# Kernel tuning notes

Hardware: AMD Instinct MI355X
Metric: run time of the kernel (lower is better)

## Reference

```python
import jax, jax.numpy as jnp
import numpy as np

BN_EPS = 1e-5
LRELU_SLOPE = 0.2  # CBL = Conv1d(k=1) + BatchNorm1d + LeakyReLU


def three_nn(xyz1, xyz2):
    # xyz1: (B,N,3), xyz2: (B,M,3) -> squared dists (B,N,3), idx (B,N,3)
    d2 = (jnp.sum(xyz1 ** 2, -1, keepdims=True)
          + jnp.sum(xyz2 ** 2, -1)[:, None, :]
          - 2.0 * jnp.einsum('bnd,bmd->bnm', xyz1, xyz2))  # (B,N,M)
    neg, idx = jax.lax.top_k(-d2, 3)
    return -neg, idx


def three_interpolate(points2, idx, weight):
    # points2: (B,C,M), idx: (B,N,3), weight: (B,N,3) -> (B,C,N)
    gathered = jax.vmap(lambda p, i: p[:, i])(points2, idx)  # (B,C,N,3)
    return jnp.einsum('bcnk,bnk->bcn', gathered, weight)


def cbl(x, W, b, gamma, beta):
    # x: (B,C,N); 1x1 conv -> BN (training-mode stats) -> LeakyReLU
    y = jnp.einsum('oc,bcn->bon', W, x) + b[None, :, None]
    mean = jnp.mean(y, axis=(0, 2), keepdims=True)
    var = jnp.var(y, axis=(0, 2), keepdims=True)
    y = (y - mean) * jax.lax.rsqrt(var + BN_EPS)
    y = gamma[None, :, None] * y + beta[None, :, None]
    return jnp.where(y >= 0, y, LRELU_SLOPE * y)


def setup_inputs() -> dict:
    key = jax.random.key(0)
    ks = jax.random.split(key, 8)
    B, N, M = 4, 8192, 2048
    C1, C2 = 128, 256
    Cin = C2 + C1  # use_points1=True -> concat
    H = 256
    return {
        'xyz1': jax.random.normal(ks[0], (B, N, 3), jnp.float32),
        'xyz2': jax.random.normal(ks[1], (B, M, 3), jnp.float32),
        'points1': jax.random.normal(ks[2], (B, C1, N), jnp.float32),
        'points2': jax.random.normal(ks[3], (B, C2, M), jnp.float32),
        'W1': jax.random.normal(ks[4], (H, Cin), jnp.float32) * (1.0 / np.sqrt(Cin)),
        'b1': jnp.zeros((H,), jnp.float32),
        'gamma1': jnp.ones((H,), jnp.float32),
        'beta1': jnp.zeros((H,), jnp.float32),
        'W2': jax.random.normal(ks[5], (H, H), jnp.float32) * (1.0 / np.sqrt(H)),
        'b2': jnp.zeros((H,), jnp.float32),
        'gamma2': jnp.ones((H,), jnp.float32),
        'beta2': jnp.zeros((H,), jnp.float32),
    }


def reference(xyz1, xyz2, points1, points2, W1, b1, gamma1, beta1, W2, b2, gamma2, beta2):
    dist, idx = three_nn(xyz1, xyz2)
    dist = jnp.maximum(dist, 1e-10)
    recip = 1.0 / dist
    weight = recip / jnp.sum(recip, axis=2, keepdims=True)  # (B,N,3)
    interp = three_interpolate(points2, idx, weight)        # (B,C2,N)
    new_points = jnp.concatenate([interp, points1], axis=1)  # (B,C2+C1,N)
    new_points = cbl(new_points, W1, b1, gamma1, beta1)
    new_points = cbl(new_points, W2, b2, gamma2, beta2)
    return new_points
```

## Files before the change

kernel.cpp:

```cpp
#include <hip/hip_runtime.h>
#include <math.h>

constexpr int B   = 4;
constexpr int N   = 8192;
constexpr int M   = 2048;
constexpr int C1  = 128;
constexpr int C2  = 256;
constexpr int HCH = 256;
constexpr int CIN = 384;
constexpr float BN_EPS = 1e-5f;
constexpr float SLOPE  = 0.2f;
constexpr float BN_CNT = (float)(B * N);

typedef __attribute__((ext_vector_type(8))) short short8;
typedef __attribute__((ext_vector_type(4))) float f32x4;

__device__ __forceinline__ unsigned short bfh(float x) {
  unsigned int u = __float_as_uint(x);
  return (unsigned short)((u + 0x7fffu + ((u >> 16) & 1u)) >> 16);
}
__device__ __forceinline__ float bf2f(unsigned short h) {
  return __uint_as_float((unsigned int)h << 16);
}
__device__ __forceinline__ unsigned int pk(unsigned short a, unsigned short b) {
  return (unsigned int)a | ((unsigned int)b << 16);
}

__global__ void k_zero(float* __restrict__ stats) {
  int i = blockIdx.x * blockDim.x + threadIdx.x;
  if (i < 1024) stats[i] = 0.f;
}

__global__ __launch_bounds__(256) void k_nn(const float* __restrict__ xyz1,
                                            const float* __restrict__ xyz2,
                                            float* __restrict__ wgt,
                                            int* __restrict__ idxo) {
  __shared__ float4 q[4][512];
  __shared__ float  md[4][64][3];
  __shared__ int    mi[4][64][3];
  const int tid = threadIdx.x;
  const int b   = blockIdx.y;
  const int n0  = blockIdx.x * 64;

  const float* src = xyz2 + (size_t)b * M * 3;
  for (int i = tid; i < M; i += 256) {
    float x = src[i*3+0], y = src[i*3+1], z = src[i*3+2];
    q[i >> 9][i & 511] = make_float4(x, y, z, x*x + y*y + z*z);
  }
  __syncthreads();

  const int w = tid >> 6;
  const int t = tid & 63;
  const int n = n0 + t;
  const float* p = xyz1 + ((size_t)b * N + n) * 3;
  const float px = p[0], py = p[1], pz = p[2];
  const float n1 = px*px + py*py + pz*pz;

  float d0 = 3.4e38f, d1 = 3.4e38f, d2 = 3.4e38f;
  int   j0 = 0, j1 = 0, j2 = 0;
  const float4* qs = q[w];
  #pragma unroll 4
  for (int r = 0; r < 512; ++r) {
    float4 c = qs[r];
    float dot = px*c.x + py*c.y + pz*c.z;
    float d = fmaf(-2.f, dot, n1 + c.w);
    if (d < d2) {
      int m = (w << 9) + r;
      if (d < d1) {
        if (d < d0) { d2 = d1; j2 = j1; d1 = d0; j1 = j0; d0 = d; j0 = m; }
        else        { d2 = d1; j2 = j1; d1 = d;  j1 = m; }
      } else        { d2 = d;  j2 = m; }
    }
  }
  md[w][t][0] = d0; md[w][t][1] = d1; md[w][t][2] = d2;
  mi[w][t][0] = j0; mi[w][t][1] = j1; mi[w][t][2] = j2;
  __syncthreads();

  if (tid < 64) {
    float e0 = 3.4e38f, e1 = 3.4e38f, e2 = 3.4e38f;
    int   i0 = 0, i1 = 0, i2 = 0;
    #pragma unroll
    for (int s = 0; s < 4; ++s) {
      #pragma unroll
      for (int k = 0; k < 3; ++k) {
        float d = md[s][tid][k];
        int   m = mi[s][tid][k];
        if (d < e2) {
          if (d < e1) {
            if (d < e0) { e2 = e1; i2 = i1; e1 = e0; i1 = i0; e0 = d; i0 = m; }
            else        { e2 = e1; i2 = i1; e1 = d;  i1 = m; }
          } else        { e2 = d;  i2 = m; }
        }
      }
    }
    e0 = fmaxf(e0, 1e-10f); e1 = fmaxf(e1, 1e-10f); e2 = fmaxf(e2, 1e-10f);
    float r0 = 1.f / e0, r1 = 1.f / e1, r2 = 1.f / e2;
    float s  = r0 + r1 + r2;
    size_t base = ((size_t)b * N + n0 + tid) * 3;
    wgt[base+0] = r0 / s;  wgt[base+1] = r1 / s;  wgt[base+2] = r2 / s;
    idxo[base+0] = i0;     idxo[base+1] = i1;     idxo[base+2] = i2;
  }
}

__global__ __launch_bounds__(256) void k_tr(const float* __restrict__ P2,
                                            float* __restrict__ P2T) {
  __shared__ float t[32][33];
  const int b  = blockIdx.z;
  const int m0 = blockIdx.x * 32;
  const int c0 = blockIdx.y * 32;
  const int tx = threadIdx.x & 31;
  const int ty = threadIdx.x >> 5;
  const float* src = P2 + (size_t)b * C2 * M;
  #pragma unroll
  for (int j = 0; j < 4; ++j)
    t[ty + j*8][tx] = src[(size_t)(c0 + ty + j*8) * M + m0 + tx];
  __syncthreads();
  float* dst = P2T + (size_t)b * M * C2;
  #pragma unroll
  for (int j = 0; j < 4; ++j)
    dst[(size_t)(m0 + ty + j*8) * C2 + c0 + tx] = t[tx][ty + j*8];
}

__global__ __launch_bounds__(256) void k_interp(const float* __restrict__ P2T,
                                                const float* __restrict__ points1,
                                                const float* __restrict__ wgt,
                                                const int* __restrict__ idx,
                                                float* __restrict__ X) {
  const int b = blockIdx.y;
  const int n = blockIdx.x * 256 + threadIdx.x;
  const size_t base = (size_t)b * N + n;
  const int i0 = idx[base*3+0], i1 = idx[base*3+1], i2 = idx[base*3+2];
  const float w0 = wgt[base*3+0], w1 = wgt[base*3+1], w2 = wgt[base*3+2];
  const float4* r0 = (const float4*)(P2T + ((size_t)b * M + i0) * C2);
  const float4* r1 = (const float4*)(P2T + ((size_t)b * M + i1) * C2);
  const float4* r2 = (const float4*)(P2T + ((size_t)b * M + i2) * C2);
  float* Xb = X + (size_t)b * CIN * N + n;
  #pragma unroll 4
  for (int c4 = 0; c4 < C2/4; ++c4) {
    float4 a0 = r0[c4], a1 = r1[c4], a2 = r2[c4];
    Xb[(size_t)(c4*4+0) * N] = w0*a0.x + w1*a1.x + w2*a2.x;
    Xb[(size_t)(c4*4+1) * N] = w0*a0.y + w1*a1.y + w2*a2.y;
    Xb[(size_t)(c4*4+2) * N] = w0*a0.z + w1*a1.z + w2*a2.z;
    Xb[(size_t)(c4*4+3) * N] = w0*a0.w + w1*a1.w + w2*a2.w;
  }
  const float* p1 = points1 + (size_t)b * C1 * N + n;
  float* Xc = Xb + (size_t)C2 * N;
  #pragma unroll 4
  for (int c = 0; c < C1; ++c) Xc[(size_t)c * N] = p1[(size_t)c * N];
}

template <int K, bool XFORM>
__global__ __launch_bounds__(256, 2) void k_gemm(const float* __restrict__ Wm,
                                                 const float* __restrict__ bias,
                                                 const float* __restrict__ Xin,
                                                 const float* __restrict__ coef,
                                                 float* __restrict__ Yout,
                                                 float* __restrict__ stats) {
  constexpr int BM = 128, BN = 128, BK = 32, RL = 40;
  __shared__ unsigned short Wh[BM*RL], Wl[BM*RL], Xh[BN*RL], Xl[BN*RL];

  const int tid = threadIdx.x;
  const int n0 = blockIdx.x * BN;
  const int o0 = blockIdx.y * BM;
  const int b  = blockIdx.z;
  const float* Xb = Xin + (size_t)b * K * N;

  const int sr = tid >> 1;
  const int kh = (tid & 1) * 16;

  const int lane = tid & 63;
  const int wv = tid >> 6;
  const int wm = wv >> 1, wn = wv & 1;
  const int lr = lane & 15;
  const int lk = (lane >> 4) * 8;

  f32x4 acc[4][4] = {};

  for (int k0 = 0; k0 < K; k0 += BK) {
    {
      const float* wp = Wm + (size_t)(o0 + sr) * K + k0 + kh;
      float xv[16];
      *(float4*)&xv[0]  = *(const float4*)(wp + 0);
      *(float4*)&xv[4]  = *(const float4*)(wp + 4);
      *(float4*)&xv[8]  = *(const float4*)(wp + 8);
      *(float4*)&xv[12] = *(const float4*)(wp + 12);
      unsigned short h[16], l[16];
      #pragma unroll
      for (int i = 0; i < 16; ++i) {
        h[i] = bfh(xv[i]);
        l[i] = bfh(xv[i] - bf2f(h[i]));
      }
      uint4* dh = (uint4*)&Wh[sr*RL + kh];
      uint4* dl = (uint4*)&Wl[sr*RL + kh];
      dh[0] = make_uint4(pk(h[0],h[1]),  pk(h[2],h[3]),  pk(h[4],h[5]),  pk(h[6],h[7]));
      dh[1] = make_uint4(pk(h[8],h[9]),  pk(h[10],h[11]),pk(h[12],h[13]),pk(h[14],h[15]));
      dl[0] = make_uint4(pk(l[0],l[1]),  pk(l[2],l[3]),  pk(l[4],l[5]),  pk(l[6],l[7]));
      dl[1] = make_uint4(pk(l[8],l[9]),  pk(l[10],l[11]),pk(l[12],l[13]),pk(l[14],l[15]));
    }
    {
      float xv[16];
      #pragma unroll
      for (int i = 0; i < 16; ++i)
        xv[i] = Xb[(size_t)(k0 + kh + i) * N + n0 + sr];
      if constexpr (XFORM) {
        #pragma unroll
        for (int i = 0; i < 16; ++i) {
          const int c = k0 + kh + i;
          float t = fmaf(coef[c], xv[i], coef[256 + c]);
          xv[i] = t >= 0.f ? t : SLOPE * t;
        }
      }
      unsigned short h[16], l[16];
      #pragma unroll
      for (int i = 0; i < 16; ++i) {
        h[i] = bfh(xv[i]);
        l[i] = bfh(xv[i] - bf2f(h[i]));
      }
      uint4* dh = (uint4*)&Xh[sr*RL + kh];
      uint4* dl = (uint4*)&Xl[sr*RL + kh];
      dh[0] = make_uint4(pk(h[0],h[1]),  pk(h[2],h[3]),  pk(h[4],h[5]),  pk(h[6],h[7]));
      dh[1] = make_uint4(pk(h[8],h[9]),  pk(h[10],h[11]),pk(h[12],h[13]),pk(h[14],h[15]));
      dl[0] = make_uint4(pk(l[0],l[1]),  pk(l[2],l[3]),  pk(l[4],l[5]),  pk(l[6],l[7]));
      dl[1] = make_uint4(pk(l[8],l[9]),  pk(l[10],l[11]),pk(l[12],l[13]),pk(l[14],l[15]));
    }
    __syncthreads();

    short8 bh[4], bl[4];
    #pragma unroll
    for (int n = 0; n < 4; ++n) {
      bh[n] = *(const short8*)&Xh[(wn*64 + n*16 + lr)*RL + lk];
      bl[n] = *(const short8*)&Xl[(wn*64 + n*16 + lr)*RL + lk];
    }
    #pragma unroll
    for (int m = 0; m < 4; ++m) {
      short8 ah = *(const short8*)&Wh[(wm*64 + m*16 + lr)*RL + lk];
      short8 al = *(const short8*)&Wl[(wm*64 + m*16 + lr)*RL + lk];
      #pragma unroll
      for (int n = 0; n < 4; ++n) {
        acc[m][n] = __builtin_amdgcn_mfma_f32_16x16x32_bf16(ah, bh[n], acc[m][n], 0, 0, 0);
        acc[m][n] = __builtin_amdgcn_mfma_f32_16x16x32_bf16(ah, bl[n], acc[m][n], 0, 0, 0);
        acc[m][n] = __builtin_amdgcn_mfma_f32_16x16x32_bf16(al, bh[n], acc[m][n], 0, 0, 0);
      }
    }
    __syncthreads();
  }

  #pragma unroll
  for (int m = 0; m < 4; ++m) {
    #pragma unroll
    for (int r = 0; r < 4; ++r) {
      const int o = o0 + wm*64 + m*16 + (lane >> 4)*4 + r;
      const float bi = bias[o];
      float s = 0.f, q = 0.f;
      #pragma unroll
      for (int n = 0; n < 4; ++n) {
        float v = acc[m][n][r] + bi;
        Yout[((size_t)b * HCH + o) * N + n0 + wn*64 + n*16 + lr] = v;
        s += v; q += v*v;
      }
      #pragma unroll
      for (int off = 1; off < 16; off <<= 1) {
        s += __shfl_xor(s, off);
        q += __shfl_xor(q, off);
      }
      if (lr == 0) {
        atomicAdd(&stats[o], s);
        atomicAdd(&stats[256 + o], q);
      }
    }
  }
}

__global__ void k_fin(const float* __restrict__ stats,
                      const float* __restrict__ gamma,
                      const float* __restrict__ beta,
                      float* __restrict__ coef) {
  const int c = threadIdx.x;
  const float mean = stats[c] / BN_CNT;
  const float var  = stats[256 + c] / BN_CNT - mean * mean;
  const float a    = gamma[c] / sqrtf(var + BN_EPS);
  coef[c]       = a;
  coef[256 + c] = fmaf(-a, mean, beta[c]);
}

__global__ __launch_bounds__(256) void k_apply(const float* __restrict__ Y,
                                               const float* __restrict__ coef,
                                               float* __restrict__ out) {
  const size_t total = (size_t)B * HCH * N / 4;
  const float4* y4 = (const float4*)Y;
  float4* o4 = (float4*)out;
  for (size_t f = (size_t)blockIdx.x * blockDim.x + threadIdx.x; f < total;
       f += (size_t)gridDim.x * blockDim.x) {
    const int c = (int)((f / (N / 4)) % HCH);
    const float a = coef[c], bb = coef[256 + c];
    float4 v = y4[f];
    float t;
    t = fmaf(a, v.x, bb); v.x = t >= 0.f ? t : SLOPE * t;
    t = fmaf(a, v.y, bb); v.y = t >= 0.f ? t : SLOPE * t;
    t = fmaf(a, v.z, bb); v.z = t >= 0.f ? t : SLOPE * t;
    t = fmaf(a, v.w, bb); v.w = t >= 0.f ? t : SLOPE * t;
    o4[f] = v;
  }
}

extern "C" void kernel_launch(void* const* d_in, const int* in_sizes, int n_in,
                              void* d_out, int out_size, void* d_ws, size_t ws_size,
                              hipStream_t stream) {
  const float* xyz1    = (const float*)d_in[0];
  const float* xyz2    = (const float*)d_in[1];
  const float* points1 = (const float*)d_in[2];
  const float* points2 = (const float*)d_in[3];
  const float* W1      = (const float*)d_in[4];
  const float* b1      = (const float*)d_in[5];
  const float* gamma1  = (const float*)d_in[6];
  const float* beta1   = (const float*)d_in[7];
  const float* W2      = (const float*)d_in[8];
  const float* b2      = (const float*)d_in[9];
  const float* gamma2  = (const float*)d_in[10];
  const float* beta2   = (const float*)d_in[11];

  float* ws = (float*)d_ws;
  float* wgt    = ws;
  int*   idx    = (int*)(ws + (size_t)B * N * 3);
  float* P2T    = ws + 2 * (size_t)B * N * 3;
  float* Xbuf   = P2T + (size_t)B * M * C2;
  float* Y1     = Xbuf + (size_t)B * CIN * N;
  float* Y2     = Xbuf;
  float* stats1 = Y1 + (size_t)B * HCH * N;
  float* stats2 = stats1 + 512;
  float* coef1  = stats2 + 512;
  float* coef2  = coef1 + 512;

  k_zero<<<4, 256, 0, stream>>>(stats1);
  k_nn<<<dim3(N / 64, B), 256, 0, stream>>>(xyz1, xyz2, wgt, idx);
  k_tr<<<dim3(M / 32, C2 / 32, B), 256, 0, stream>>>(points2, P2T);
  k_interp<<<dim3(N / 256, B), 256, 0, stream>>>(P2T, points1, wgt, idx, Xbuf);
  k_gemm<CIN, false><<<dim3(N / 128, HCH / 128, B), 256, 0, stream>>>(W1, b1, Xbuf, nullptr, Y1, stats1);
  k_fin<<<1, 256, 0, stream>>>(stats1, gamma1, beta1, coef1);
  k_gemm<HCH, true><<<dim3(N / 128, HCH / 128, B), 256, 0, stream>>>(W2, b2, Y1, coef1, Y2, stats2);
  k_fin<<<1, 256, 0, stream>>>(stats2, gamma2, beta2, coef2);
  k_apply<<<2048, 256, 0, stream>>>(Y2, coef2, (float*)d_out);
}
```

Measured before the change: 399.5 us.

## Pre-split GEMM operands to bf16 hi/lo in N-major layout outside the GEMM

```diff
diff --git a/kernel.cpp b/kernel.cpp
--- a/kernel.cpp
+++ b/kernel.cpp
@@ -125,48 +125,116 @@
                                                 const float* __restrict__ points1,
                                                 const float* __restrict__ wgt,
                                                 const int* __restrict__ idx,
-                                                float* __restrict__ X) {
-  const int b = blockIdx.y;
-  const int n = blockIdx.x * 256 + threadIdx.x;
+                                                unsigned short* __restrict__ Xh,
+                                                unsigned short* __restrict__ Xl) {
+  const int tid = threadIdx.x;
+  const int q   = tid >> 6;
+  const int b   = blockIdx.y;
+  const int n   = blockIdx.x * 64 + (tid & 63);
   const size_t base = (size_t)b * N + n;
   const int i0 = idx[base*3+0], i1 = idx[base*3+1], i2 = idx[base*3+2];
   const float w0 = wgt[base*3+0], w1 = wgt[base*3+1], w2 = wgt[base*3+2];
-  const float4* r0 = (const float4*)(P2T + ((size_t)b * M + i0) * C2);
-  const float4* r1 = (const float4*)(P2T + ((size_t)b * M + i1) * C2);
-  const float4* r2 = (const float4*)(P2T + ((size_t)b * M + i2) * C2);
-  float* Xb = X + (size_t)b * CIN * N + n;
+  const float4* r0 = (const float4*)(P2T + ((size_t)b * M + i0) * C2) + q*16;
+  const float4* r1 = (const float4*)(P2T + ((size_t)b * M + i1) * C2) + q*16;
+  const float4* r2 = (const float4*)(P2T + ((size_t)b * M + i2) * C2) + q*16;
+  unsigned short* rh = Xh + base * CIN;
+  unsigned short* rl = Xl + base * CIN;
+
   #pragma unroll 4
-  for (int c4 = 0; c4 < C2/4; ++c4) {
+  for (int c4 = 0; c4 < 16; ++c4) {
     float4 a0 = r0[c4], a1 = r1[c4], a2 = r2[c4];
-    Xb[(size_t)(c4*4+0) * N] = w0*a0.x + w1*a1.x + w2*a2.x;
-    Xb[(size_t)(c4*4+1) * N] = w0*a0.y + w1*a1.y + w2*a2.y;
-    Xb[(size_t)(c4*4+2) * N] = w0*a0.z + w1*a1.z + w2*a2.z;
-    Xb[(size_t)(c4*4+3) * N] = w0*a0.w + w1*a1.w + w2*a2.w;
-  }
-  const float* p1 = points1 + (size_t)b * C1 * N + n;
-  float* Xc = Xb + (size_t)C2 * N;
+    float v0 = w0*a0.x + w1*a1.x + w2*a2.x;
+    float v1 = w0*a0.y + w1*a1.y + w2*a2.y;
+    float v2 = w0*a0.z + w1*a1.z + w2*a2.z;
+    float v3 = w0*a0.w + w1*a1.w + w2*a2.w;
+    unsigned short h0=bfh(v0), h1=bfh(v1), h2=bfh(v2), h3=bfh(v3);
+    uint2 sh; sh.x = pk(h0,h1); sh.y = pk(h2,h3);
+    uint2 sl; sl.x = pk(bfh(v0-bf2f(h0)), bfh(v1-bf2f(h1)));
+              sl.y = pk(bfh(v2-bf2f(h2)), bfh(v3-bf2f(h3)));
+    *(uint2*)&rh[q*64 + c4*4] = sh;
+    *(uint2*)&rl[q*64 + c4*4] = sl;
+  }
+  const float* p1 = points1 + ((size_t)b * C1 + q*32) * N + n;
   #pragma unroll 4
-  for (int c = 0; c < C1; ++c) Xc[(size_t)c * N] = p1[(size_t)c * N];
-}
-
-template <int K, bool XFORM>
-__global__ __launch_bounds__(256, 2) void k_gemm(const float* __restrict__ Wm,
+  for (int j = 0; j < 32; j += 4) {
+    float v0 = p1[(size_t)(j+0) * N];
+    float v1 = p1[(size_t)(j+1) * N];
+    float v2 = p1[(size_t)(j+2) * N];
+    float v3 = p1[(size_t)(j+3) * N];
+    unsigned short h0=bfh(v0), h1=bfh(v1), h2=bfh(v2), h3=bfh(v3);
+    uint2 sh; sh.x = pk(h0,h1); sh.y = pk(h2,h3);
+    uint2 sl; sl.x = pk(bfh(v0-bf2f(h0)), bfh(v1-bf2f(h1)));
+              sl.y = pk(bfh(v2-bf2f(h2)), bfh(v3-bf2f(h3)));
+    *(uint2*)&rh[256 + q*32 + j] = sh;
+    *(uint2*)&rl[256 + q*32 + j] = sl;
+  }
+}
+
+__global__ void k_split(const float* __restrict__ src,
+                        unsigned short* __restrict__ h,
+                        unsigned short* __restrict__ l, int n) {
+  int i = blockIdx.x * 256 + threadIdx.x;
+  if (i < n) {
+    float v = src[i];
+    unsigned short hh = bfh(v);
+    h[i] = hh;
+    l[i] = bfh(v - bf2f(hh));
+  }
+}
+
+__global__ __launch_bounds__(256) void k_mid(const float* __restrict__ Y1,
+                                             const float* __restrict__ coef,
+                                             unsigned short* __restrict__ Th,
+                                             unsigned short* __restrict__ Tl) {
+  __shared__ float T[32][33];
+  const int b  = blockIdx.z;
+  const int n0 = blockIdx.x * 32;
+  const int o0 = blockIdx.y * 32;
+  const int tx = threadIdx.x & 31;
+  const int ty = threadIdx.x >> 5;
+  #pragma unroll
+  for (int j = 0; j < 4; ++j) {
+    const int o = o0 + ty + j*8;
+    const float a = coef[o], bb = coef[256 + o];
+    float t = fmaf(a, Y1[((size_t)b * HCH + o) * N + n0 + tx], bb);
+    T[ty + j*8][tx] = t >= 0.f ? t : SLOPE * t;
+  }
+  __syncthreads();
+  const int r = threadIdx.x >> 3;
+  const int u = threadIdx.x & 7;
+  const size_t ro = ((size_t)b * N + n0 + r) * HCH + o0;
+  #pragma unroll
+  for (int uu = u; uu < 16; uu += 8) {
+    float v0 = T[uu*2][r], v1 = T[uu*2+1][r];
+    unsigned short h0 = bfh(v0), h1 = bfh(v1);
+    ((unsigned int*)&Th[ro])[uu] = pk(h0, h1);
+    ((unsigned int*)&Tl[ro])[uu] = pk(bfh(v0 - bf2f(h0)), bfh(v1 - bf2f(h1)));
+  }
+}
+
+template <int K>
+__global__ __launch_bounds__(256, 4) void k_gemm(const unsigned short* __restrict__ Wh,
+                                                 const unsigned short* __restrict__ Wl,
                                                  const float* __restrict__ bias,
-                                                 const float* __restrict__ Xin,
-                                                 const float* __restrict__ coef,
+                                                 const unsigned short* __restrict__ Xh,
+                                                 const unsigned short* __restrict__ Xl,
                                                  float* __restrict__ Yout,
                                                  float* __restrict__ stats) {
-  constexpr int BM = 128, BN = 128, BK = 32, RL = 40;
-  __shared__ unsigned short Wh[BM*RL], Wl[BM*RL], Xh[BN*RL], Xl[BN*RL];
+  constexpr int RL = 40;
+  __shared__ unsigned short Whs[64*RL], Wls[64*RL], Xhs[128*RL], Xls[128*RL];
 
   const int tid = threadIdx.x;
-  const int n0 = blockIdx.x * BN;
-  const int o0 = blockIdx.y * BM;
+  const int n0 = blockIdx.x * 128;
+  const int o0 = blockIdx.y * 64;
   const int b  = blockIdx.z;
-  const float* Xb = Xin + (size_t)b * K * N;
-
-  const int sr = tid >> 1;
-  const int kh = (tid & 1) * 16;
+
+  const int srw = tid >> 2, kq = (tid & 3) * 8;
+  const int srx = tid >> 1, kh = (tid & 1) * 16;
+
+  const unsigned short* WhP = Wh + (size_t)(o0 + srw) * K;
+  const unsigned short* WlP = Wl + (size_t)(o0 + srw) * K;
+  const unsigned short* XhP = Xh + ((size_t)b * N + n0 + srx) * K;
+  const unsigned short* XlP = Xl + ((size_t)b * N + n0 + srx) * K;
 
   const int lane = tid & 63;
   const int wv = tid >> 6;
@@ -174,98 +242,61 @@
   const int lr = lane & 15;
   const int lk = (lane >> 4) * 8;
 
-  f32x4 acc[4][4] = {};
-
-  for (int k0 = 0; k0 < K; k0 += BK) {
-    {
-      const float* wp = Wm + (size_t)(o0 + sr) * K + k0 + kh;
-      float xv[16];
-      *(float4*)&xv[0]  = *(const float4*)(wp + 0);
-      *(float4*)&xv[4]  = *(const float4*)(wp + 4);
-      *(float4*)&xv[8]  = *(const float4*)(wp + 8);
-      *(float4*)&xv[12] = *(const float4*)(wp + 12);
-      unsigned short h[16], l[16];
-      #pragma unroll
-      for (int i = 0; i < 16; ++i) {
-        h[i] = bfh(xv[i]);
-        l[i] = bfh(xv[i] - bf2f(h[i]));
-      }
-      uint4* dh = (uint4*)&Wh[sr*RL + kh];
-      uint4* dl = (uint4*)&Wl[sr*RL + kh];
-      dh[0] = make_uint4(pk(h[0],h[1]),  pk(h[2],h[3]),  pk(h[4],h[5]),  pk(h[6],h[7]));
-      dh[1] = make_uint4(pk(h[8],h[9]),  pk(h[10],h[11]),pk(h[12],h[13]),pk(h[14],h[15]));
-      dl[0] = make_uint4(pk(l[0],l[1]),  pk(l[2],l[3]),  pk(l[4],l[5]),  pk(l[6],l[7]));
-      dl[1] = make_uint4(pk(l[8],l[9]),  pk(l[10],l[11]),pk(l[12],l[13]),pk(l[14],l[15]));
-    }
-    {
-      float xv[16];
-      #pragma unroll
-      for (int i = 0; i < 16; ++i)
-        xv[i] = Xb[(size_t)(k0 + kh + i) * N + n0 + sr];
-      if constexpr (XFORM) {
-        #pragma unroll
-        for (int i = 0; i < 16; ++i) {
-          const int c = k0 + kh + i;
-          float t = fmaf(coef[c], xv[i], coef[256 + c]);
-          xv[i] = t >= 0.f ? t : SLOPE * t;
-        }
-      }
-      unsigned short h[16], l[16];
-      #pragma unroll
-      for (int i = 0; i < 16; ++i) {
-        h[i] = bfh(xv[i]);
-        l[i] = bfh(xv[i] - bf2f(h[i]));
-      }
-      uint4* dh = (uint4*)&Xh[sr*RL + kh];
-      uint4* dl = (uint4*)&Xl[sr*RL + kh];
-      dh[0] = make_uint4(pk(h[0],h[1]),  pk(h[2],h[3]),  pk(h[4],h[5]),  pk(h[6],h[7]));
-      dh[1] = make_uint4(pk(h[8],h[9]),  pk(h[10],h[11]),pk(h[12],h[13]),pk(h[14],h[15]));
-      dl[0] = make_uint4(pk(l[0],l[1]),  pk(l[2],l[3]),  pk(l[4],l[5]),  pk(l[6],l[7]));
-      dl[1] = make_uint4(pk(l[8],l[9]),  pk(l[10],l[11]),pk(l[12],l[13]),pk(l[14],l[15]));
-    }
+  f32x4 acc[2][4] = {};
+
+  for (int k0 = 0; k0 < K; k0 += 32) {
+    *(uint4*)&Whs[srw*RL + kq]     = *(const uint4*)&WhP[k0 + kq];
+    *(uint4*)&Wls[srw*RL + kq]     = *(const uint4*)&WlP[k0 + kq];
+    *(uint4*)&Xhs[srx*RL + kh]     = *(const uint4*)&XhP[k0 + kh];
+    *(uint4*)&Xhs[srx*RL + kh + 8] = *(const uint4*)&XhP[k0 + kh + 8];
+    *(uint4*)&Xls[srx*RL + kh]     = *(const uint4*)&XlP[k0 + kh];
+    *(uint4*)&Xls[srx*RL + kh + 8] = *(const uint4*)&XlP[k0 + kh + 8];
     __syncthreads();
 
-    short8 bh[4], bl[4];
+    short8 bh[4], bl[4], ah[2], al[2];
     #pragma unroll
     for (int n = 0; n < 4; ++n) {
-      bh[n] = *(const short8*)&Xh[(wn*64 + n*16 + lr)*RL + lk];
-      bl[n] = *(const short8*)&Xl[(wn*64 + n*16 + lr)*RL + lk];
-    }
-    #pragma unroll
-    for (int m = 0; m < 4; ++m) {
-      short8 ah = *(const short8*)&Wh[(wm*64 + m*16 + lr)*RL + lk];
-      short8 al = *(const short8*)&Wl[(wm*64 + m*16 + lr)*RL + lk];
+      bh[n] = *(const short8*)&Xhs[(wn*64 + n*16 + lr)*RL + lk];
+      bl[n] = *(const short8*)&Xls[(wn*64 + n*16 + lr)*RL + lk];
+    }
+    #pragma unroll
+    for (int m = 0; m < 2; ++m) {
+      ah[m] = *(const short8*)&Whs[(wm*32 + m*16 + lr)*RL + lk];
+      al[m] = *(const short8*)&Wls[(wm*32 + m*16 + lr)*RL + lk];
+    }
+    #pragma unroll
+    for (int m = 0; m < 2; ++m) {
       #pragma unroll
       for (int n = 0; n < 4; ++n) {
-        acc[m][n] = __builtin_amdgcn_mfma_f32_16x16x32_bf16(ah, bh[n], acc[m][n], 0, 0, 0);
-        acc[m][n] = __builtin_amdgcn_mfma_f32_16x16x32_bf16(ah, bl[n], acc[m][n], 0, 0, 0);
-        acc[m][n] = __builtin_amdgcn_mfma_f32_16x16x32_bf16(al, bh[n], acc[m][n], 0, 0, 0);
+        acc[m][n] = __builtin_amdgcn_mfma_f32_16x16x32_bf16(ah[m], bh[n], acc[m][n], 0, 0, 0);
+        acc[m][n] = __builtin_amdgcn_mfma_f32_16x16x32_bf16(ah[m], bl[n], acc[m][n], 0, 0, 0);
+        acc[m][n] = __builtin_amdgcn_mfma_f32_16x16x32_bf16(al[m], bh[n], acc[m][n], 0, 0, 0);
       }
     }
     __syncthreads();
   }
 
   #pragma unroll
-  for (int m = 0; m < 4; ++m) {
+  for (int m = 0; m < 2; ++m) {
     #pragma unroll
     for (int r = 0; r < 4; ++r) {
-      const int o = o0 + wm*64 + m*16 + (lane >> 4)*4 + r;
+      const int o = o0 + wm*32 + m*16 + (lane >> 4)*4 + r;
       const float bi = bias[o];
-      float s = 0.f, q = 0.f;
+      float s = 0.f, qq = 0.f;
       #pragma unroll
       for (int n = 0; n < 4; ++n) {
         float v = acc[m][n][r] + bi;
         Yout[((size_t)b * HCH + o) * N + n0 + wn*64 + n*16 + lr] = v;
-        s += v; q += v*v;
+        s += v; qq += v*v;
       }
       #pragma unroll
       for (int off = 1; off < 16; off <<= 1) {
-        s += __shfl_xor(s, off);
-        q += __shfl_xor(q, off);
+        s  += __shfl_xor(s, off);
+        qq += __shfl_xor(qq, off);
       }
       if (lr == 0) {
         atomicAdd(&stats[o], s);
-        atomicAdd(&stats[256 + o], q);
+        atomicAdd(&stats[256 + o], qq);
       }
     }
   }
@@ -319,25 +350,35 @@
   const float* gamma2  = (const float*)d_in[10];
   const float* beta2   = (const float*)d_in[11];
 
-  float* ws = (float*)d_ws;
-  float* wgt    = ws;
-  int*   idx    = (int*)(ws + (size_t)B * N * 3);
-  float* P2T    = ws + 2 * (size_t)B * N * 3;
-  float* Xbuf   = P2T + (size_t)B * M * C2;
-  float* Y1     = Xbuf + (size_t)B * CIN * N;
-  float* Y2     = Xbuf;
-  float* stats1 = Y1 + (size_t)B * HCH * N;
-  float* stats2 = stats1 + 512;
-  float* coef1  = stats2 + 512;
-  float* coef2  = coef1 + 512;
+  char* w = (char*)d_ws;
+  float* wgt            = (float*)w;                         w += (size_t)B*N*3*4;
+  int*   idx            = (int*)w;                           w += (size_t)B*N*3*4;
+  float* P2T            = (float*)w;                         w += (size_t)B*M*C2*4;
+  float* Y1             = (float*)w;                         w += (size_t)B*HCH*N*4;
+  unsigned short* XhT   = (unsigned short*)w;                w += (size_t)B*N*CIN*2;
+  unsigned short* XlT   = (unsigned short*)w;                w += (size_t)B*N*CIN*2;
+  unsigned short* W1h   = (unsigned short*)w;                w += (size_t)HCH*CIN*2;
+  unsigned short* W1l   = (unsigned short*)w;                w += (size_t)HCH*CIN*2;
+  unsigned short* W2h   = (unsigned short*)w;                w += (size_t)HCH*HCH*2;
+  unsigned short* W2l   = (unsigned short*)w;                w += (size_t)HCH*HCH*2;
+  float* stats1         = (float*)w;                         w += 512*4;
+  float* stats2         = (float*)w;                         w += 512*4;
+  float* coef1          = (float*)w;                         w += 512*4;
+  float* coef2          = (float*)w;                         w += 512*4;
+  float* Y2             = Y1;
+  unsigned short* Y1hT  = XhT;
+  unsigned short* Y1lT  = XlT;
 
   k_zero<<<4, 256, 0, stream>>>(stats1);
   k_nn<<<dim3(N / 64, B), 256, 0, stream>>>(xyz1, xyz2, wgt, idx);
   k_tr<<<dim3(M / 32, C2 / 32, B), 256, 0, stream>>>(points2, P2T);
-  k_interp<<<dim3(N / 256, B), 256, 0, stream>>>(P2T, points1, wgt, idx, Xbuf);
-  k_gemm<CIN, false><<<dim3(N / 128, HCH / 128, B), 256, 0, stream>>>(W1, b1, Xbuf, nullptr, Y1, stats1);
+  k_interp<<<dim3(N / 64, B), 256, 0, stream>>>(P2T, points1, wgt, idx, XhT, XlT);
+  k_split<<<(HCH*CIN + 255) / 256, 256, 0, stream>>>(W1, W1h, W1l, HCH*CIN);
+  k_split<<<(HCH*HCH + 255) / 256, 256, 0, stream>>>(W2, W2h, W2l, HCH*HCH);
+  k_gemm<CIN><<<dim3(N / 128, HCH / 64, B), 256, 0, stream>>>(W1h, W1l, b1, XhT, XlT, Y1, stats1);
   k_fin<<<1, 256, 0, stream>>>(stats1, gamma1, beta1, coef1);
-  k_gemm<HCH, true><<<dim3(N / 128, HCH / 128, B), 256, 0, stream>>>(W2, b2, Y1, coef1, Y2, stats2);
+  k_mid<<<dim3(N / 32, HCH / 32, B), 256, 0, stream>>>(Y1, coef1, Y1hT, Y1lT);
+  k_gemm<HCH><<<dim3(N / 128, HCH / 64, B), 256, 0, stream>>>(W2h, W2l, b2, Y1hT, Y1lT, Y2, stats2);
   k_fin<<<1, 256, 0, stream>>>(stats2, gamma2, beta2, coef2);
   k_apply<<<2048, 256, 0, stream>>>(Y2, coef2, (float*)d_out);
 }
```

Measured after the change: 404.2 us. About the same (+1.2%).
